# Kernel optimization log

Hardware: AMD Instinct MI355X
Metric: run time of the kernel (lower is better)

The kernel has to match this reference:

```python
import jax, jax.numpy as jnp
import numpy as np

R = 16
ALPHA = 32
SCALING = ALPHA / R  # 2.0


def setup_inputs() -> dict:
    key = jax.random.key(0)
    k_x, k_w, k_b, k_a, k_bm = jax.random.split(key, 5)
    d = 1024
    x = jax.random.normal(k_x, (4, 4096, d), dtype=jnp.float32)
    W = jax.random.normal(k_w, (d, d), dtype=jnp.float32) * 0.02
    b = jax.random.normal(k_b, (d,), dtype=jnp.float32) * 0.02
    A = jax.random.normal(k_a, (R, d), dtype=jnp.float32) * 0.02
    B = jax.random.normal(k_bm, (d, R), dtype=jnp.float32) * 0.02
    return {"x": x, "W": W, "b": b, "A": A, "B": B}


def reference(x, W, b, A, B):
    # base linear: x @ W^T + b   (W: [out, in])
    base = jnp.einsum("bsd,od->bso", x, W) + b
    # low-rank update: (x @ A^T) @ B^T, scaled (dropout p=0 -> identity)
    u = jnp.einsum("bsd,rd->bsr", x, A)   # [B, S, r]
    update = jnp.einsum("bsr,or->bso", u, B)
    return base + SCALING * update
```

## Files before the change

### kernel.cpp

```cpp
#include <hip/hip_runtime.h>


typedef __bf16 bf16x8 __attribute__((ext_vector_type(8)));
typedef float f32x4 __attribute__((ext_vector_type(4)));
typedef unsigned short ushort8 __attribute__((ext_vector_type(8)));

__device__ __forceinline__ unsigned short f2bf(float f) {
    __bf16 h = (__bf16)f;
    union { __bf16 b; unsigned short u; } v; v.b = h; return v.u;
}
__device__ __forceinline__ ushort8 cvt8(f32x4 a, f32x4 b) {
    ushort8 o;
#pragma unroll
    for (int i = 0; i < 4; ++i) { o[i] = f2bf(a[i]); o[i + 4] = f2bf(b[i]); }
    return o;
}
__device__ __forceinline__ void gld16(const unsigned short* g, unsigned short* l) {
    __builtin_amdgcn_global_load_lds(
        (const __attribute__((address_space(1))) unsigned int*)g,
        (__attribute__((address_space(3))) unsigned int*)l, 16, 0, 0);
}

__global__ __launch_bounds__(256) void prep(
    const float* __restrict__ X, const float* __restrict__ W,
    const float* __restrict__ A, const float* __restrict__ B,
    unsigned short* __restrict__ xbf, unsigned short* __restrict__ Weff)
{
    const int b = blockIdx.x;
    if (b < 512) {
        const int idx = b * 256 + threadIdx.x;
        const int o  = idx >> 7;
        const int kc = (idx & 127) << 3;
        float br[16];
#pragma unroll
        for (int r = 0; r < 16; ++r) br[r] = 2.0f * B[o * 16 + r];
        float acc[8];
        const float* wrow = W + (size_t)o * 1024 + kc;
#pragma unroll
        for (int j = 0; j < 8; ++j) acc[j] = wrow[j];
#pragma unroll
        for (int r = 0; r < 16; ++r) {
            const float* arow = A + r * 1024 + kc;
#pragma unroll
            for (int j = 0; j < 8; ++j) acc[j] += br[r] * arow[j];
        }
        ushort8 o8;
#pragma unroll
        for (int j = 0; j < 8; ++j) o8[j] = f2bf(acc[j]);
        *(ushort8*)(Weff + (size_t)o * 1024 + kc) = o8;
    } else {
        const size_t i = ((size_t)(b - 512) * 256 + threadIdx.x) * 8;
        f32x4 a = *(const f32x4*)(X + i);
        f32x4 c = *(const f32x4*)(X + i + 4);
        *(ushort8*)(xbf + i) = cvt8(a, c);
    }
}

template <bool XF32>
__global__ __launch_bounds__(256) void gemm_bt(
    const void* __restrict__ X_,
    const unsigned short* __restrict__ Wt,
    const float* __restrict__ bias,
    float* __restrict__ out)
{
    __shared__ __align__(16) unsigned short lA[128 * 32];
    __shared__ __align__(16) unsigned short lB[128 * 32];

    const int t    = threadIdx.x;
    const int lane = t & 63;
    const int w    = t >> 6;
    const int bm   = blockIdx.x * 128;
    const int bn   = blockIdx.y * 128;
    const int wm   = (w & 1) * 64;
    const int wn   = (w >> 1) * 64;
    const int r16  = lane & 15;
    const int quad = lane >> 4;

    const int srow = t >> 2;
    const int gc   = (t & 3) ^ ((srow >> 1) & 3);
    unsigned short* lsA = lA + t * 8;
    unsigned short* lsB = lB + t * 8;
    const size_t ga0 = (size_t)(bm + srow) * 1024 + gc * 8;
    const size_t ga1 = (size_t)(bm + srow + 64) * 1024 + gc * 8;
    const unsigned short* gB0 = Wt + (size_t)(bn + srow) * 1024 + gc * 8;

    const int p    = (quad ^ ((r16 >> 1) & 3)) * 8;
    const int aoff = (wm + r16) * 32 + p;
    const int boff = (wn + r16) * 32 + p;

    const unsigned short* Xb = (const unsigned short*)X_;
    const float*          Xf = (const float*)X_;

    f32x4 acc[4][4];
#pragma unroll
    for (int i = 0; i < 4; ++i)
#pragma unroll
        for (int j = 0; j < 4; ++j) {
            f32x4 z = {0.f, 0.f, 0.f, 0.f};
            acc[i][j] = z;
        }

    for (int kt = 0; kt < 1024; kt += 32) {
        if (XF32) {
            f32x4 a0 = *(const f32x4*)(Xf + ga0 + kt);
            f32x4 a1 = *(const f32x4*)(Xf + ga0 + kt + 4);
            f32x4 a2 = *(const f32x4*)(Xf + ga1 + kt);
            f32x4 a3 = *(const f32x4*)(Xf + ga1 + kt + 4);
            *(ushort8*)lsA          = cvt8(a0, a1);
            *(ushort8*)(lsA + 2048) = cvt8(a2, a3);
        } else {
            gld16(Xb + ga0 + kt, lsA);
            gld16(Xb + ga1 + kt, lsA + 2048);
        }
        gld16(gB0 + kt,             lsB);
        gld16(gB0 + kt + 64 * 1024, lsB + 2048);
        __syncthreads();

        bf16x8 fa[4], fb[4];
#pragma unroll
        for (int mt = 0; mt < 4; ++mt) fa[mt] = *(const bf16x8*)(lA + aoff + mt * 16 * 32);
#pragma unroll
        for (int nt = 0; nt < 4; ++nt) fb[nt] = *(const bf16x8*)(lB + boff + nt * 16 * 32);

#pragma unroll
        for (int mt = 0; mt < 4; ++mt)
#pragma unroll
            for (int nt = 0; nt < 4; ++nt)
                acc[mt][nt] = __builtin_amdgcn_mfma_f32_16x16x32_bf16(
                    fa[mt], fb[nt], acc[mt][nt], 0, 0, 0);

        __syncthreads();
    }

    const int orow0 = bm + wm + quad * 4;
    const int ocol0 = bn + wn + r16;
#pragma unroll
    for (int nt = 0; nt < 4; ++nt) {
        const float bv = bias[ocol0 + nt * 16];
#pragma unroll
        for (int mt = 0; mt < 4; ++mt)
#pragma unroll
            for (int i = 0; i < 4; ++i)
                out[(size_t)(orow0 + mt * 16 + i) * 1024 + (ocol0 + nt * 16)] =
                    acc[mt][nt][i] + bv;
    }
}

extern "C" void kernel_launch(void* const* d_in, const int* in_sizes, int n_in,
                              void* d_out, int out_size, void* d_ws, size_t ws_size,
                              hipStream_t stream) {
    const float* x  = (const float*)d_in[0];
    const float* W  = (const float*)d_in[1];
    const float* b  = (const float*)d_in[2];
    const float* A  = (const float*)d_in[3];
    const float* Bm = (const float*)d_in[4];
    float* out = (float*)d_out;

    const int M = in_sizes[0] / 1024;
    dim3 grid(M / 128, 1024 / 128);

    const bool fast = ws_size >= ((size_t)(M)*1024*2 + (2u << 20) + 4096);
    if (fast) {
        unsigned short* xbf  = (unsigned short*)d_ws;
        unsigned short* Weff = xbf + (size_t)M * 1024;
        hipLaunchKernelGGL(prep, dim3(512 + M / 2), dim3(256), 0, stream,
                           x, W, A, Bm, xbf, Weff);
        hipLaunchKernelGGL((gemm_bt<false>), grid, dim3(256), 0, stream,
                           (const void*)xbf, Weff, b, out);
    } else {
        unsigned short* Weff = (unsigned short*)d_ws;
        hipLaunchKernelGGL(prep, dim3(512), dim3(256), 0, stream,
                           x, W, A, Bm, (unsigned short*)nullptr, Weff);
        hipLaunchKernelGGL((gemm_bt<true>), grid, dim3(256), 0, stream,
                           (const void*)x, Weff, b, out);
    }
}
```

Before: 165.6 us.

## Double-buffer LDS tiles to overlap next K-tile loads with MFMA compute

Splits the A and B shared-memory tiles into ping-pong buffers and prefetches the first K tile before the loop. Each iteration then issues the next tile's global-to-LDS loads before running the current tile's MFMAs, and one barrier per iteration replaces two. The aim is to hide global load latency behind compute, at the cost of twice the LDS use, which may lower occupancy. Correctness depends on the async global_load_lds having completed at the barrier.

```diff
diff --git a/kernel.cpp b/kernel.cpp
--- a/kernel.cpp
+++ b/kernel.cpp
@@ -6,8 +6,7 @@
 typedef unsigned short ushort8 __attribute__((ext_vector_type(8)));
 
 __device__ __forceinline__ unsigned short f2bf(float f) {
-    __bf16 h = (__bf16)f;
-    union { __bf16 b; unsigned short u; } v; v.b = h; return v.u;
+    union { __bf16 b; unsigned short u; } v; v.b = (__bf16)f; return v.u;
 }
 __device__ __forceinline__ ushort8 cvt8(f32x4 a, f32x4 b) {
     ushort8 o;
@@ -63,8 +62,10 @@
     const float* __restrict__ bias,
     float* __restrict__ out)
 {
-    __shared__ __align__(16) unsigned short lA[128 * 32];
-    __shared__ __align__(16) unsigned short lB[128 * 32];
+    __shared__ __align__(16) unsigned short lA0[128 * 32];
+    __shared__ __align__(16) unsigned short lA1[128 * 32];
+    __shared__ __align__(16) unsigned short lB0[128 * 32];
+    __shared__ __align__(16) unsigned short lB1[128 * 32];
 
     const int t    = threadIdx.x;
     const int lane = t & 63;
@@ -78,8 +79,6 @@
 
     const int srow = t >> 2;
     const int gc   = (t & 3) ^ ((srow >> 1) & 3);
-    unsigned short* lsA = lA + t * 8;
-    unsigned short* lsB = lB + t * 8;
     const size_t ga0 = (size_t)(bm + srow) * 1024 + gc * 8;
     const size_t ga1 = (size_t)(bm + srow + 64) * 1024 + gc * 8;
     const unsigned short* gB0 = Wt + (size_t)(bn + srow) * 1024 + gc * 8;
@@ -100,27 +99,47 @@
             acc[i][j] = z;
         }
 
+    unsigned short* sA  = lA0;  unsigned short* sAn = lA1;
+    unsigned short* sB  = lB0;  unsigned short* sBn = lB1;
+
+    if (XF32) {
+        f32x4 a0 = *(const f32x4*)(Xf + ga0);
+        f32x4 a1 = *(const f32x4*)(Xf + ga0 + 4);
+        f32x4 a2 = *(const f32x4*)(Xf + ga1);
+        f32x4 a3 = *(const f32x4*)(Xf + ga1 + 4);
+        *(ushort8*)(sA + t * 8)        = cvt8(a0, a1);
+        *(ushort8*)(sA + 2048 + t * 8) = cvt8(a2, a3);
+    } else {
+        gld16(Xb + ga0, sA + t * 8);
+        gld16(Xb + ga1, sA + 2048 + t * 8);
+    }
+    gld16(gB0,             sB + t * 8);
+    gld16(gB0 + 64 * 1024, sB + 2048 + t * 8);
+    __syncthreads();
+
     for (int kt = 0; kt < 1024; kt += 32) {
-        if (XF32) {
-            f32x4 a0 = *(const f32x4*)(Xf + ga0 + kt);
-            f32x4 a1 = *(const f32x4*)(Xf + ga0 + kt + 4);
-            f32x4 a2 = *(const f32x4*)(Xf + ga1 + kt);
-            f32x4 a3 = *(const f32x4*)(Xf + ga1 + kt + 4);
-            *(ushort8*)lsA          = cvt8(a0, a1);
-            *(ushort8*)(lsA + 2048) = cvt8(a2, a3);
-        } else {
-            gld16(Xb + ga0 + kt, lsA);
-            gld16(Xb + ga1 + kt, lsA + 2048);
+        if (kt + 32 < 1024) {
+            const int kn = kt + 32;
+            if (XF32) {
+                f32x4 a0 = *(const f32x4*)(Xf + ga0 + kn);
+                f32x4 a1 = *(const f32x4*)(Xf + ga0 + kn + 4);
+                f32x4 a2 = *(const f32x4*)(Xf + ga1 + kn);
+                f32x4 a3 = *(const f32x4*)(Xf + ga1 + kn + 4);
+                *(ushort8*)(sAn + t * 8)        = cvt8(a0, a1);
+                *(ushort8*)(sAn + 2048 + t * 8) = cvt8(a2, a3);
+            } else {
+                gld16(Xb + ga0 + kn, sAn + t * 8);
+                gld16(Xb + ga1 + kn, sAn + 2048 + t * 8);
+            }
+            gld16(gB0 + kn,             sBn + t * 8);
+            gld16(gB0 + kn + 64 * 1024, sBn + 2048 + t * 8);
         }
-        gld16(gB0 + kt,             lsB);
-        gld16(gB0 + kt + 64 * 1024, lsB + 2048);
-        __syncthreads();
 
         bf16x8 fa[4], fb[4];
 #pragma unroll
-        for (int mt = 0; mt < 4; ++mt) fa[mt] = *(const bf16x8*)(lA + aoff + mt * 16 * 32);
+        for (int mt = 0; mt < 4; ++mt) fa[mt] = *(const bf16x8*)(sA + aoff + mt * 16 * 32);
 #pragma unroll
-        for (int nt = 0; nt < 4; ++nt) fb[nt] = *(const bf16x8*)(lB + boff + nt * 16 * 32);
+        for (int nt = 0; nt < 4; ++nt) fb[nt] = *(const bf16x8*)(sB + boff + nt * 16 * 32);
 
 #pragma unroll
         for (int mt = 0; mt < 4; ++mt)
@@ -129,6 +148,9 @@
                 acc[mt][nt] = __builtin_amdgcn_mfma_f32_16x16x32_bf16(
                     fa[mt], fb[nt], acc[mt][nt], 0, 0, 0);
 
+        unsigned short* tp;
+        tp = sA; sA = sAn; sAn = tp;
+        tp = sB; sB = sBn; sBn = tp;
         __syncthreads();
     }
 
```

Result: no change. 168.4 us (+1.7%).

## Load MFMA fragments directly from global memory with register prefetch, dropping LDS

Applied to the files above, without the earlier changes.

The GEMM no longer stages tiles through shared memory. Each lane loads its bf16 MFMA fragments straight from global memory and prefetches the next k-step into registers, which removes both __syncthreads per iteration. The cost is that each wave now loads its own A and B rows with no sharing inside the block, so global and L2 traffic rises (each operand is fetched twice per block). The strided per-lane 16-byte row accesses also coalesce less well.

```diff
diff --git a/kernel.cpp b/kernel.cpp
--- a/kernel.cpp
+++ b/kernel.cpp
@@ -6,8 +6,7 @@
 typedef unsigned short ushort8 __attribute__((ext_vector_type(8)));
 
 __device__ __forceinline__ unsigned short f2bf(float f) {
-    __bf16 h = (__bf16)f;
-    union { __bf16 b; unsigned short u; } v; v.b = h; return v.u;
+    union { __bf16 b; unsigned short u; } v; v.b = (__bf16)f; return v.u;
 }
 __device__ __forceinline__ ushort8 cvt8(f32x4 a, f32x4 b) {
     ushort8 o;
@@ -15,10 +14,8 @@
     for (int i = 0; i < 4; ++i) { o[i] = f2bf(a[i]); o[i + 4] = f2bf(b[i]); }
     return o;
 }
-__device__ __forceinline__ void gld16(const unsigned short* g, unsigned short* l) {
-    __builtin_amdgcn_global_load_lds(
-        (const __attribute__((address_space(1))) unsigned int*)g,
-        (__attribute__((address_space(3))) unsigned int*)l, 16, 0, 0);
+__device__ __forceinline__ bf16x8 cvtfrag(f32x4 a, f32x4 b) {
+    union { ushort8 u; bf16x8 h; } v; v.u = cvt8(a, b); return v.h;
 }
 
 __global__ __launch_bounds__(256) void prep(
@@ -57,15 +54,12 @@
 }
 
 template <bool XF32>
-__global__ __launch_bounds__(256) void gemm_bt(
+__global__ __launch_bounds__(256) void gemm_direct(
     const void* __restrict__ X_,
     const unsigned short* __restrict__ Wt,
     const float* __restrict__ bias,
     float* __restrict__ out)
 {
-    __shared__ __align__(16) unsigned short lA[128 * 32];
-    __shared__ __align__(16) unsigned short lB[128 * 32];
-
     const int t    = threadIdx.x;
     const int lane = t & 63;
     const int w    = t >> 6;
@@ -76,20 +70,21 @@
     const int r16  = lane & 15;
     const int quad = lane >> 4;
 
-    const int srow = t >> 2;
-    const int gc   = (t & 3) ^ ((srow >> 1) & 3);
-    unsigned short* lsA = lA + t * 8;
-    unsigned short* lsB = lB + t * 8;
-    const size_t ga0 = (size_t)(bm + srow) * 1024 + gc * 8;
-    const size_t ga1 = (size_t)(bm + srow + 64) * 1024 + gc * 8;
-    const unsigned short* gB0 = Wt + (size_t)(bn + srow) * 1024 + gc * 8;
-
-    const int p    = (quad ^ ((r16 >> 1) & 3)) * 8;
-    const int aoff = (wm + r16) * 32 + p;
-    const int boff = (wn + r16) * 32 + p;
-
     const unsigned short* Xb = (const unsigned short*)X_;
     const float*          Xf = (const float*)X_;
+
+    const unsigned short* rowA[4];
+    const float*          rowAf[4];
+    const unsigned short* rowB[4];
+#pragma unroll
+    for (int mt = 0; mt < 4; ++mt) {
+        const size_t r = (size_t)(bm + wm + mt * 16 + r16) * 1024 + quad * 8;
+        rowA[mt]  = Xb + r;
+        rowAf[mt] = Xf + r;
+    }
+#pragma unroll
+    for (int nt = 0; nt < 4; ++nt)
+        rowB[nt] = Wt + (size_t)(bn + wn + nt * 16 + r16) * 1024 + quad * 8;
 
     f32x4 acc[4][4];
 #pragma unroll
@@ -100,27 +95,26 @@
             acc[i][j] = z;
         }
 
+    bf16x8 fa[4], fb[4], na[4], nb[4];
+#pragma unroll
+    for (int mt = 0; mt < 4; ++mt)
+        fa[mt] = XF32 ? cvtfrag(*(const f32x4*)(rowAf[mt]),
+                                *(const f32x4*)(rowAf[mt] + 4))
+                      : *(const bf16x8*)(rowA[mt]);
+#pragma unroll
+    for (int nt = 0; nt < 4; ++nt) fb[nt] = *(const bf16x8*)(rowB[nt]);
+
     for (int kt = 0; kt < 1024; kt += 32) {
-        if (XF32) {
-            f32x4 a0 = *(const f32x4*)(Xf + ga0 + kt);
-            f32x4 a1 = *(const f32x4*)(Xf + ga0 + kt + 4);
-            f32x4 a2 = *(const f32x4*)(Xf + ga1 + kt);
-            f32x4 a3 = *(const f32x4*)(Xf + ga1 + kt + 4);
-            *(ushort8*)lsA          = cvt8(a0, a1);
-            *(ushort8*)(lsA + 2048) = cvt8(a2, a3);
-        } else {
-            gld16(Xb + ga0 + kt, lsA);
-            gld16(Xb + ga1 + kt, lsA + 2048);
+        const int kn = kt + 32;
+        if (kn < 1024) {
+#pragma unroll
+            for (int mt = 0; mt < 4; ++mt)
+                na[mt] = XF32 ? cvtfrag(*(const f32x4*)(rowAf[mt] + kn),
+                                        *(const f32x4*)(rowAf[mt] + kn + 4))
+                              : *(const bf16x8*)(rowA[mt] + kn);
+#pragma unroll
+            for (int nt = 0; nt < 4; ++nt) nb[nt] = *(const bf16x8*)(rowB[nt] + kn);
         }
-        gld16(gB0 + kt,             lsB);
-        gld16(gB0 + kt + 64 * 1024, lsB + 2048);
-        __syncthreads();
-
-        bf16x8 fa[4], fb[4];
-#pragma unroll
-        for (int mt = 0; mt < 4; ++mt) fa[mt] = *(const bf16x8*)(lA + aoff + mt * 16 * 32);
-#pragma unroll
-        for (int nt = 0; nt < 4; ++nt) fb[nt] = *(const bf16x8*)(lB + boff + nt * 16 * 32);
 
 #pragma unroll
         for (int mt = 0; mt < 4; ++mt)
@@ -129,7 +123,10 @@
                 acc[mt][nt] = __builtin_amdgcn_mfma_f32_16x16x32_bf16(
                     fa[mt], fb[nt], acc[mt][nt], 0, 0, 0);
 
-        __syncthreads();
+#pragma unroll
+        for (int mt = 0; mt < 4; ++mt) fa[mt] = na[mt];
+#pragma unroll
+        for (int nt = 0; nt < 4; ++nt) fb[nt] = nb[nt];
     }
 
     const int orow0 = bm + wm + quad * 4;
@@ -165,13 +162,13 @@
         unsigned short* Weff = xbf + (size_t)M * 1024;
         hipLaunchKernelGGL(prep, dim3(512 + M / 2), dim3(256), 0, stream,
                            x, W, A, Bm, xbf, Weff);
-        hipLaunchKernelGGL((gemm_bt<false>), grid, dim3(256), 0, stream,
+        hipLaunchKernelGGL((gemm_direct<false>), grid, dim3(256), 0, stream,
                            (const void*)xbf, Weff, b, out);
     } else {
         unsigned short* Weff = (unsigned short*)d_ws;
         hipLaunchKernelGGL(prep, dim3(512), dim3(256), 0, stream,
                            x, W, A, Bm, (unsigned short*)nullptr, Weff);
-        hipLaunchKernelGGL((gemm_bt<true>), grid, dim3(256), 0, stream,
+        hipLaunchKernelGGL((gemm_direct<true>), grid, dim3(256), 0, stream,
                            (const void*)x, Weff, b, out);
     }
 }
```

Result: slower. 234.4 us (+41.5%).

## Replace 4-wave 128x128 GEMM tile with single-wave 64x64 blocks

Applied to the files above, without the earlier changes.

The GEMM kernel moves from 256-thread blocks computing 128x128 tiles to 64-thread single-wavefront blocks computing 64x64 tiles, launching four times as many blocks. Each wave now loads its own A and B tiles into LDS. The aim is more blocks in flight and less barrier cost across waves. In exchange, each loaded byte is reused half as much, so global and L2 traffic per output roughly doubles.

```diff
diff --git a/kernel.cpp b/kernel.cpp
--- a/kernel.cpp
+++ b/kernel.cpp
@@ -6,8 +6,7 @@
 typedef unsigned short ushort8 __attribute__((ext_vector_type(8)));
 
 __device__ __forceinline__ unsigned short f2bf(float f) {
-    __bf16 h = (__bf16)f;
-    union { __bf16 b; unsigned short u; } v; v.b = h; return v.u;
+    union { __bf16 b; unsigned short u; } v; v.b = (__bf16)f; return v.u;
 }
 __device__ __forceinline__ ushort8 cvt8(f32x4 a, f32x4 b) {
     ushort8 o;
@@ -57,39 +56,37 @@
 }
 
 template <bool XF32>
-__global__ __launch_bounds__(256) void gemm_bt(
+__global__ __launch_bounds__(64, 4) void gemm_w64(
     const void* __restrict__ X_,
     const unsigned short* __restrict__ Wt,
     const float* __restrict__ bias,
     float* __restrict__ out)
 {
-    __shared__ __align__(16) unsigned short lA[128 * 32];
-    __shared__ __align__(16) unsigned short lB[128 * 32];
+    __shared__ __align__(16) unsigned short lA[64 * 32];
+    __shared__ __align__(16) unsigned short lB[64 * 32];
 
-    const int t    = threadIdx.x;
-    const int lane = t & 63;
-    const int w    = t >> 6;
-    const int bm   = blockIdx.x * 128;
-    const int bn   = blockIdx.y * 128;
-    const int wm   = (w & 1) * 64;
-    const int wn   = (w >> 1) * 64;
+    const int lane = threadIdx.x;
+    const int bm   = blockIdx.x * 64;
+    const int bn   = blockIdx.y * 64;
     const int r16  = lane & 15;
     const int quad = lane >> 4;
-
-    const int srow = t >> 2;
-    const int gc   = (t & 3) ^ ((srow >> 1) & 3);
-    unsigned short* lsA = lA + t * 8;
-    unsigned short* lsB = lB + t * 8;
-    const size_t ga0 = (size_t)(bm + srow) * 1024 + gc * 8;
-    const size_t ga1 = (size_t)(bm + srow + 64) * 1024 + gc * 8;
-    const unsigned short* gB0 = Wt + (size_t)(bn + srow) * 1024 + gc * 8;
-
-    const int p    = (quad ^ ((r16 >> 1) & 3)) * 8;
-    const int aoff = (wm + r16) * 32 + p;
-    const int boff = (wn + r16) * 32 + p;
+    const int sr   = lane >> 2;
+    const int gc   = (lane & 3) ^ ((sr >> 1) & 3);
 
     const unsigned short* Xb = (const unsigned short*)X_;
     const float*          Xf = (const float*)X_;
+
+    size_t gA[4], gB[4];
+#pragma unroll
+    for (int j = 0; j < 4; ++j) {
+        gA[j] = (size_t)(bm + j * 16 + sr) * 1024 + gc * 8;
+        gB[j] = (size_t)(bn + j * 16 + sr) * 1024 + gc * 8;
+    }
+    unsigned short* const lsA = lA + lane * 8;
+    unsigned short* const lsB = lB + lane * 8;
+
+    const int p    = (quad ^ ((r16 >> 1) & 3)) * 8;
+    const int aoff = r16 * 32 + p;
 
     f32x4 acc[4][4];
 #pragma unroll
@@ -102,25 +99,27 @@
 
     for (int kt = 0; kt < 1024; kt += 32) {
         if (XF32) {
-            f32x4 a0 = *(const f32x4*)(Xf + ga0 + kt);
-            f32x4 a1 = *(const f32x4*)(Xf + ga0 + kt + 4);
-            f32x4 a2 = *(const f32x4*)(Xf + ga1 + kt);
-            f32x4 a3 = *(const f32x4*)(Xf + ga1 + kt + 4);
-            *(ushort8*)lsA          = cvt8(a0, a1);
-            *(ushort8*)(lsA + 2048) = cvt8(a2, a3);
+#pragma unroll
+            for (int j = 0; j < 4; ++j) {
+                f32x4 a0 = *(const f32x4*)(Xf + gA[j] + kt);
+                f32x4 a1 = *(const f32x4*)(Xf + gA[j] + kt + 4);
+                *(ushort8*)(lsA + j * 512) = cvt8(a0, a1);
+                gld16(Wt + gB[j] + kt, lsB + j * 512);
+            }
         } else {
-            gld16(Xb + ga0 + kt, lsA);
-            gld16(Xb + ga1 + kt, lsA + 2048);
+#pragma unroll
+            for (int j = 0; j < 4; ++j) {
+                gld16(Xb + gA[j] + kt, lsA + j * 512);
+                gld16(Wt + gB[j] + kt, lsB + j * 512);
+            }
         }
-        gld16(gB0 + kt,             lsB);
-        gld16(gB0 + kt + 64 * 1024, lsB + 2048);
         __syncthreads();
 
         bf16x8 fa[4], fb[4];
 #pragma unroll
         for (int mt = 0; mt < 4; ++mt) fa[mt] = *(const bf16x8*)(lA + aoff + mt * 16 * 32);
 #pragma unroll
-        for (int nt = 0; nt < 4; ++nt) fb[nt] = *(const bf16x8*)(lB + boff + nt * 16 * 32);
+        for (int nt = 0; nt < 4; ++nt) fb[nt] = *(const bf16x8*)(lB + aoff - (r16*32+p) + (bn*0) + (nt * 16 + r16) * 32 + p);
 
 #pragma unroll
         for (int mt = 0; mt < 4; ++mt)
@@ -132,8 +131,8 @@
         __syncthreads();
     }
 
-    const int orow0 = bm + wm + quad * 4;
-    const int ocol0 = bn + wn + r16;
+    const int orow0 = bm + quad * 4;
+    const int ocol0 = bn + r16;
 #pragma unroll
     for (int nt = 0; nt < 4; ++nt) {
         const float bv = bias[ocol0 + nt * 16];
@@ -157,7 +156,7 @@
     float* out = (float*)d_out;
 
     const int M = in_sizes[0] / 1024;
-    dim3 grid(M / 128, 1024 / 128);
+    dim3 grid(M / 64, 1024 / 64);
 
     const bool fast = ws_size >= ((size_t)(M)*1024*2 + (2u << 20) + 4096);
     if (fast) {
@@ -165,13 +164,13 @@
         unsigned short* Weff = xbf + (size_t)M * 1024;
         hipLaunchKernelGGL(prep, dim3(512 + M / 2), dim3(256), 0, stream,
                            x, W, A, Bm, xbf, Weff);
-        hipLaunchKernelGGL((gemm_bt<false>), grid, dim3(256), 0, stream,
+        hipLaunchKernelGGL((gemm_w64<false>), grid, dim3(64), 0, stream,
                            (const void*)xbf, Weff, b, out);
     } else {
         unsigned short* Weff = (unsigned short*)d_ws;
         hipLaunchKernelGGL(prep, dim3(512), dim3(256), 0, stream,
                            x, W, A, Bm, (unsigned short*)nullptr, Weff);
-        hipLaunchKernelGGL((gemm_bt<true>), grid, dim3(256), 0, stream,
+        hipLaunchKernelGGL((gemm_w64<true>), grid, dim3(64), 0, stream,
                            (const void*)x, Weff, b, out);
     }
 }
```

Measured after the change: 174.4 us. 1.05x slower.
